# Kernel optimization log

Hardware: AMD Instinct MI355X
Metric: run time of the kernel (lower is better)

## Reference

```python
import math
import jax, jax.numpy as jnp
import numpy as np

B, K, D, R = 8192, 64, 128, 8
EPSILON = 1.0  # alpha_scale, used as diffusion epsilon


def setup_inputs() -> dict:
    key = jax.random.key(0)
    k1, k2, k3 = jax.random.split(key, 3)
    y = jax.random.normal(k1, (B, D), dtype=jnp.float32)
    m = 0.2 * jax.random.normal(k2, (K, D), dtype=jnp.float32)          # init_mean_scale=0.2
    delta = jnp.full((K, D), -2.0, dtype=jnp.float32)                    # init_delta=-2.0
    U = 0.001 * jax.random.normal(k3, (K, D, R), dtype=jnp.float32)
    # log_alpha_raw = alpha_scale * log(ones(K)/K)
    log_alpha_raw = jnp.full((K,), math.log(1.0 / K), dtype=jnp.float32)
    return {"y": y, "m": m, "delta": delta, "U": U, "log_alpha_raw": log_alpha_raw}


def reference(y, m, delta, U, log_alpha_raw):
    """log z_theta(y) = logsumexp_k [log_alpha_k + log N(y; m_k, eps*S_k)],
    S_k = diag(exp(delta_k)) + U_k U_k^T, solved via Woodbury + Cholesky."""
    d = y.shape[-1]
    eps = jnp.asarray(EPSILON, y.dtype)
    log_alpha = (log_alpha_raw - jnp.mean(log_alpha_raw)) / EPSILON

    S_diag = jnp.exp(delta)            # [K, d]
    S_inv = 1.0 / S_diag               # [K, d]

    # Capacitance M_k = I_r + U_k^T diag(S_inv_k) U_k, Cholesky L_k
    V = S_inv[..., None] * U                              # [K, d, r]
    Mcap = jnp.eye(R, dtype=y.dtype) + jnp.einsum('kdr,kds->krs', U, V)  # [K, r, r]
    L = jnp.linalg.cholesky(Mcap)                         # [K, r, r]
    logdet_S = jnp.sum(jnp.log(S_diag), axis=-1) \
        + 2.0 * jnp.sum(jnp.log(jnp.diagonal(L, axis1=-2, axis2=-1)), axis=-1)  # [K]

    diff = y[:, None, :] - m[None, :, :]                  # [B, K, d]
    u1 = diff * S_inv[None]                               # [B, K, d]
    # Woodbury correction: solve M_k s = U_k^T u1 for all (b, k)
    t = jnp.einsum('kdr,bkd->krb', U, u1)                 # [K, r, B] (B as multiple RHS)
    z1 = jax.scipy.linalg.solve_triangular(L, t, lower=True)
    s = jax.scipy.linalg.solve_triangular(jnp.swapaxes(L, -1, -2), z1, lower=False)  # [K, r, B]
    Us = jnp.einsum('kdr,krb->bkd', U, s)                 # [B, K, d]
    S_inv_diff = u1 - Us * S_inv[None]                    # [B, K, d]

    quad = jnp.sum(diff * S_inv_diff, axis=-1)            # [B, K]
    log_norm = 0.5 * (d * (math.log(2.0 * math.pi) + jnp.log(eps)) + logdet_S)  # [K]
    logits = log_alpha[None, :] - 0.5 * quad / eps - log_norm[None, :]          # [B, K]
    return jax.scipy.special.logsumexp(logits, axis=-1)   # [B]
```

## Files before the change

### kernel.cpp

```cpp
#include <hip/hip_runtime.h>
#include <math.h>

#define D_DIM 128
#define K_DIM 64
#define R_DIM 8
#define B_DIM 8192
#define XSTR  264

#define WS_C0F   81920

typedef __bf16 bf16x8 __attribute__((ext_vector_type(8)));
typedef float  f32x4  __attribute__((ext_vector_type(4)));

static __device__ inline unsigned short f2bf(float f) {
  union { float f; unsigned int u; } v; v.f = f;
  unsigned int u = v.u;
  unsigned int lsb = (u >> 16) & 1;
  u += 0x7fffu + lsb;
  return (unsigned short)(u >> 16);
}

__global__ __launch_bounds__(128) void precomp_kernel(
    const float* __restrict__ m, const float* __restrict__ delta,
    const float* __restrict__ U, const float* __restrict__ lar,
    float* __restrict__ ws) {
  const int k = blockIdx.x;
  const int d = threadIdx.x;

  __shared__ float U_l[D_DIM][R_DIM];
  __shared__ float V_l[D_DIM][R_DIM];
  __shared__ float W_l[D_DIM][R_DIM];
  __shared__ float m_l[D_DIM];
  __shared__ float red[64];
  __shared__ float Linv_s[R_DIM][R_DIM];
  __shared__ float q_s[R_DIM];
  __shared__ float c0_s[1];
  __shared__ float redA[D_DIM], redB[D_DIM], redC[D_DIM];

  const float dl    = delta[k * D_DIM + d];
  const float s_inv = expf(-dl);
  const float mv    = m[k * D_DIM + d];
  m_l[d] = mv;
  const float* Up = U + (size_t)(k * D_DIM + d) * R_DIM;
#pragma unroll
  for (int r = 0; r < R_DIM; ++r) {
    float u = Up[r];
    U_l[d][r] = u;
    V_l[d][r] = u * s_inv;
  }
  redA[d] = dl;
  redB[d] = mv * mv * s_inv;
  redC[d] = (d < K_DIM) ? lar[d] : 0.f;
  __syncthreads();

  if (d < 64) {
    const int r = d >> 3, s = d & 7;
    float acc = (r == s) ? 1.0f : 0.0f;
#pragma unroll 8
    for (int dd = 0; dd < D_DIM; ++dd) acc += U_l[dd][r] * V_l[dd][s];
    red[d] = acc;
  }
  __syncthreads();

  for (int off = 64; off > 0; off >>= 1) {
    if (d < off) {
      redA[d] += redA[d + off];
      redB[d] += redB[d + off];
      redC[d] += redC[d + off];
    }
    __syncthreads();
  }

  if (d == 0) {
    float Lm[8][8];
#pragma unroll
    for (int i = 0; i < 8; ++i) {
#pragma unroll
      for (int j = 0; j < 8; ++j) {
        if (j > i) continue;
        float sum = red[i * 8 + j];
#pragma unroll
        for (int p = 0; p < 8; ++p)
          if (p < j) sum -= Lm[i][p] * Lm[j][p];
        if (i == j) Lm[i][i] = sqrtf(sum);
        else        Lm[i][j] = sum / Lm[j][j];
      }
    }
    float ld = 0.f;
#pragma unroll
    for (int i = 0; i < 8; ++i) ld += logf(Lm[i][i]);

    float Li[8][8];
#pragma unroll
    for (int i = 0; i < 8; ++i)
#pragma unroll
      for (int j = 0; j < 8; ++j) Li[i][j] = 0.f;
#pragma unroll
    for (int j = 0; j < 8; ++j) {
      Li[j][j] = 1.0f / Lm[j][j];
#pragma unroll
      for (int i = 0; i < 8; ++i) {
        if (i <= j) continue;
        float sum = 0.f;
#pragma unroll
        for (int p = 0; p < 8; ++p)
          if (p >= j && p < i) sum += Lm[i][p] * Li[p][j];
        Li[i][j] = -sum / Lm[i][i];
      }
    }
#pragma unroll
    for (int i = 0; i < 8; ++i)
#pragma unroll
      for (int j = 0; j < 8; ++j) Linv_s[i][j] = Li[i][j];

    const float mean = redC[0] * (1.0f / K_DIM);
    const float log_alpha = lar[k] - mean;
    const float logdetS = redA[0] + 2.0f * ld;
    const float LOG2PI = 1.8378770664093453f;
    const float log_norm = 0.5f * ((float)D_DIM * LOG2PI + logdetS);
    c0_s[0] = log_alpha - log_norm - 0.5f * redB[0];
  }
  __syncthreads();

  float Wr[R_DIM];
#pragma unroll
  for (int r = 0; r < R_DIM; ++r) {
    float acc = 0.f;
#pragma unroll
    for (int s2 = 0; s2 < R_DIM; ++s2)
      if (s2 <= r) acc += V_l[d][s2] * Linv_s[r][s2];
    Wr[r] = acc;
    W_l[d][r] = acc;
  }
  __syncthreads();

  if (d < R_DIM) {
    float acc = 0.f;
#pragma unroll 8
    for (int dd = 0; dd < D_DIM; ++dd) acc += W_l[dd][d] * m_l[dd];
    q_s[d] = acc;
  }
  __syncthreads();

  float hp = mv * s_inv;
#pragma unroll
  for (int r = 0; r < R_DIM; ++r) hp -= q_s[r] * Wr[r];

  const float INV_SQRT2 = 0.70710678118654752f;
  unsigned short* T = (unsigned short*)ws;
  const int kg = k >> 4, kl = k & 15;
  const int chunk = d >> 5, pos = d & 31;
  const size_t base_y = (((size_t)kg * 8 + chunk) * 160) * 32;
  const size_t base_q = (((size_t)kg * 8 + 4 + chunk) * 160) * 32;
#pragma unroll
  for (int c = 0; c < 8; ++c) {
    T[base_y + (size_t)(kl * 10 + c) * 32 + pos] = f2bf(Wr[c] * INV_SQRT2);
    T[base_q + (size_t)(kl * 10 + c) * 32 + pos] = 0;
  }
  T[base_y + (size_t)(kl * 10 + 8) * 32 + pos] = f2bf(hp);
  T[base_q + (size_t)(kl * 10 + 8) * 32 + pos] = f2bf(-0.5f * s_inv);
  T[base_y + (size_t)(kl * 10 + 9) * 32 + pos] = 0;
  T[base_q + (size_t)(kl * 10 + 9) * 32 + pos] = 0;

  if (d == 0) {
    float qq = 0.f;
#pragma unroll
    for (int r = 0; r < R_DIM; ++r) qq += q_s[r] * q_s[r];
    ws[WS_C0F + k] = c0_s[0] + 0.5f * qq;
  }
}

__global__ __launch_bounds__(512, 1) void logz_full(
    const float* __restrict__ y, const float* __restrict__ ws,
    float* __restrict__ out) {
  __shared__ __align__(16) char smem[16896 + 81920];
  __shared__ float vals2[32 * 65];

  unsigned short* sX = (unsigned short*)smem;
  unsigned short* sT = (unsigned short*)(smem + 16896);

  const int tid   = threadIdx.x;
  const int lane  = tid & 63;
  const int wv    = tid >> 6;
  const int wr    = wv & 1;
  const int wc    = wv >> 1;
  const int col_l = lane & 15;
  const int quad  = lane >> 4;
  const int r0    = (int)blockIdx.x * 32;

  const int kg_m = wv >> 1;
  const int wi5  = (wv & 1) * 5;

  {
#pragma unroll
    for (int j = 0; j < 5; ++j) {
      const int within = wi5 + j;
      const float* src = ws + (size_t)kg_m * 20480 + 0 * 2560 + within * 256;
      __builtin_amdgcn_global_load_lds(
          (const __attribute__((address_space(1))) void*)(src + lane * 4),
          (__attribute__((address_space(3))) void*)(sT + kg_m * 5120 + within * 512),
          16, 0, 0);
    }
  }

  {
#pragma unroll
    for (int j = 0; j < 2; ++j) {
      const int idx = tid + j * 512;
      const int row = idx >> 5, g = idx & 31;
      const float4* ya = (const float4*)y + (size_t)(r0 + row) * 32 + (g & 15) * 2;
      float4 a = ya[0], b = ya[1];
      if (g >= 16) {
        a.x *= a.x; a.y *= a.y; a.z *= a.z; a.w *= a.w;
        b.x *= b.x; b.y *= b.y; b.z *= b.z; b.w *= b.w;
      }
      union { unsigned short us[8]; uint4 v; } o;
      o.us[0] = f2bf(a.x); o.us[1] = f2bf(a.y); o.us[2] = f2bf(a.z); o.us[3] = f2bf(a.w);
      o.us[4] = f2bf(b.x); o.us[5] = f2bf(b.y); o.us[6] = f2bf(b.z); o.us[7] = f2bf(b.w);
      *(uint4*)(sX + row * XSTR + g * 8) = o.v;
    }
  }

  f32x4 acc[10];
#pragma unroll
  for (int f = 0; f < 10; ++f) { acc[f][0] = 0.f; acc[f][1] = 0.f; acc[f][2] = 0.f; acc[f][3] = 0.f; }

  const int rowA = wr * 16 + col_l;

  for (int c = 0; c < 8; ++c) {
    __syncthreads();
    if (c < 7) {
      const int nb = (c + 1) & 1;
#pragma unroll
      for (int j = 0; j < 5; ++j) {
        const int within = wi5 + j;
        const float* src = ws + (size_t)kg_m * 20480 + (c + 1) * 2560 + within * 256;
        __builtin_amdgcn_global_load_lds(
            (const __attribute__((address_space(1))) void*)(src + lane * 4),
            (__attribute__((address_space(3))) void*)(sT + nb * 20480 + kg_m * 5120 + within * 512),
            16, 0, 0);
      }
    }
    const bf16x8 a = *(const bf16x8*)(sX + rowA * XSTR + c * 32 + quad * 8);
    const unsigned short* tb = sT + (c & 1) * 20480 + wc * 5120;
#pragma unroll
    for (int f = 0; f < 10; ++f) {
      const bf16x8 b = *(const bf16x8*)(tb + (f * 16 + col_l) * 32 + quad * 8);
      acc[f] = __builtin_amdgcn_mfma_f32_16x16x32_bf16(a, b, acc[f], 0, 0, 0);
    }
  }

  __syncthreads();
  float* evals = (float*)smem;
#pragma unroll
  for (int f = 0; f < 10; ++f) {
    const int c_in = f * 16 + col_l;
    const int c10  = c_in % 10;
    const int col  = wc * 160 + c_in;
#pragma unroll
    for (int reg = 0; reg < 4; ++reg) {
      const int row = wr * 16 + quad * 4 + reg;
      const float v = acc[f][reg];
      evals[row * 640 + col] = (c10 == 8) ? v : v * v;
    }
  }
  __syncthreads();

  const float* c0p = ws + WS_C0F;
#pragma unroll
  for (int j = 0; j < 4; ++j) {
    const int idx = tid + j * 512;
    const int row = idx >> 6, kl = idx & 63;
    const float* e = evals + row * 640 + kl * 10;
    float s = c0p[kl] + e[8];
#pragma unroll
    for (int c = 0; c < 8; ++c) s += e[c];
    vals2[row * 65 + kl] = s;
  }
  __syncthreads();

#pragma unroll
  for (int rr = 0; rr < 4; ++rr) {
    const int row = wv * 4 + rr;
    const float val = vals2[row * 65 + lane];
    float mx = val;
#pragma unroll
    for (int off = 1; off < 64; off <<= 1)
      mx = fmaxf(mx, __shfl_xor(mx, off, 64));
    float ex = expf(val - mx);
#pragma unroll
    for (int off = 1; off < 64; off <<= 1)
      ex += __shfl_xor(ex, off, 64);
    if (lane == 0) out[r0 + row] = mx + logf(ex);
  }
}

extern "C" void kernel_launch(void* const* d_in, const int* in_sizes, int n_in,
                              void* d_out, int out_size, void* d_ws, size_t ws_size,
                              hipStream_t stream) {
  const float* y     = (const float*)d_in[0];
  const float* m     = (const float*)d_in[1];
  const float* delta = (const float*)d_in[2];
  const float* U     = (const float*)d_in[3];
  const float* lar   = (const float*)d_in[4];
  float* out = (float*)d_out;
  float* ws  = (float*)d_ws;

  precomp_kernel<<<K_DIM, 128, 0, stream>>>(m, delta, U, lar, ws);
  logz_full<<<B_DIM / 32, 512, 0, stream>>>(y, ws, out);
}
```

Baseline: 80.37 us.

## Reorder precomputed B-operand so each MFMA tile holds one feature across 16 components

The precomputed bf16 operand table is relaid out so that each 16-column MFMA fragment holds the same feature (one of 8 projections or the linear term) for 16 mixture components, and the zero padding columns are removed (9 fragments instead of 10). This lets each lane combine squares and the linear term directly in registers, which removes the LDS scatter of the full evaluation matrix, one barrier, and the per-component reduction pass. It also cuts global-to-LDS staging traffic and the MFMA count. The trade-off is a more irregular load loop, with 36 segments spread over 8 waves, so some waves issue an extra load.

```diff
diff --git a/kernel.cpp b/kernel.cpp
--- a/kernel.cpp
+++ b/kernel.cpp
@@ -7,7 +7,7 @@
 #define B_DIM 8192
 #define XSTR  264
 
-#define WS_C0F   81920
+#define WS_C0F   73728
 
 typedef __bf16 bf16x8 __attribute__((ext_vector_type(8)));
 typedef float  f32x4  __attribute__((ext_vector_type(4)));
@@ -150,17 +150,15 @@
   unsigned short* T = (unsigned short*)ws;
   const int kg = k >> 4, kl = k & 15;
   const int chunk = d >> 5, pos = d & 31;
-  const size_t base_y = (((size_t)kg * 8 + chunk) * 160) * 32;
-  const size_t base_q = (((size_t)kg * 8 + 4 + chunk) * 160) * 32;
-#pragma unroll
-  for (int c = 0; c < 8; ++c) {
-    T[base_y + (size_t)(kl * 10 + c) * 32 + pos] = f2bf(Wr[c] * INV_SQRT2);
-    T[base_q + (size_t)(kl * 10 + c) * 32 + pos] = 0;
-  }
-  T[base_y + (size_t)(kl * 10 + 8) * 32 + pos] = f2bf(hp);
-  T[base_q + (size_t)(kl * 10 + 8) * 32 + pos] = f2bf(-0.5f * s_inv);
-  T[base_y + (size_t)(kl * 10 + 9) * 32 + pos] = 0;
-  T[base_q + (size_t)(kl * 10 + 9) * 32 + pos] = 0;
+  const size_t by = (((size_t)(kg * 8 + chunk) * 9) * 16 + kl) * 32 + pos;
+  const size_t bq = (((size_t)(kg * 8 + chunk + 4) * 9) * 16 + kl) * 32 + pos;
+#pragma unroll
+  for (int cc = 0; cc < 8; ++cc) {
+    T[by + (size_t)cc * 512] = f2bf(Wr[cc] * INV_SQRT2);
+    T[bq + (size_t)cc * 512] = 0;
+  }
+  T[by + 8 * 512] = f2bf(hp);
+  T[bq + 8 * 512] = f2bf(-0.5f * s_inv);
 
   if (d == 0) {
     float qq = 0.f;
@@ -173,8 +171,8 @@
 __global__ __launch_bounds__(512, 1) void logz_full(
     const float* __restrict__ y, const float* __restrict__ ws,
     float* __restrict__ out) {
-  __shared__ __align__(16) char smem[16896 + 81920];
-  __shared__ float vals2[32 * 65];
+  __shared__ __align__(16) char smem[16896 + 2 * 36864];
+  __shared__ float vals2[32 * 66];
 
   unsigned short* sX = (unsigned short*)smem;
   unsigned short* sT = (unsigned short*)(smem + 16896);
@@ -188,19 +186,13 @@
   const int quad  = lane >> 4;
   const int r0    = (int)blockIdx.x * 32;
 
-  const int kg_m = wv >> 1;
-  const int wi5  = (wv & 1) * 5;
-
-  {
-#pragma unroll
-    for (int j = 0; j < 5; ++j) {
-      const int within = wi5 + j;
-      const float* src = ws + (size_t)kg_m * 20480 + 0 * 2560 + within * 256;
-      __builtin_amdgcn_global_load_lds(
-          (const __attribute__((address_space(1))) void*)(src + lane * 4),
-          (__attribute__((address_space(3))) void*)(sT + kg_m * 5120 + within * 512),
-          16, 0, 0);
-    }
+  for (int mm = wv; mm < 36; mm += 8) {
+    const int kgm = mm / 9, seg = mm - kgm * 9;
+    const float* src = ws + (size_t)(kgm * 8 + 0) * 2304 + seg * 256 + lane * 4;
+    __builtin_amdgcn_global_load_lds(
+        (const __attribute__((address_space(1))) void*)src,
+        (__attribute__((address_space(3))) void*)(sT + (kgm * 9 + seg) * 512),
+        16, 0, 0);
   }
 
   {
@@ -221,9 +213,9 @@
     }
   }
 
-  f32x4 acc[10];
-#pragma unroll
-  for (int f = 0; f < 10; ++f) { acc[f][0] = 0.f; acc[f][1] = 0.f; acc[f][2] = 0.f; acc[f][3] = 0.f; }
+  f32x4 acc[9];
+#pragma unroll
+  for (int f = 0; f < 9; ++f) { acc[f][0] = 0.f; acc[f][1] = 0.f; acc[f][2] = 0.f; acc[f][3] = 0.f; }
 
   const int rowA = wr * 16 + col_l;
 
@@ -231,58 +223,38 @@
     __syncthreads();
     if (c < 7) {
       const int nb = (c + 1) & 1;
-#pragma unroll
-      for (int j = 0; j < 5; ++j) {
-        const int within = wi5 + j;
-        const float* src = ws + (size_t)kg_m * 20480 + (c + 1) * 2560 + within * 256;
+      for (int mm = wv; mm < 36; mm += 8) {
+        const int kgm = mm / 9, seg = mm - kgm * 9;
+        const float* src = ws + (size_t)(kgm * 8 + c + 1) * 2304 + seg * 256 + lane * 4;
         __builtin_amdgcn_global_load_lds(
-            (const __attribute__((address_space(1))) void*)(src + lane * 4),
-            (__attribute__((address_space(3))) void*)(sT + nb * 20480 + kg_m * 5120 + within * 512),
+            (const __attribute__((address_space(1))) void*)src,
+            (__attribute__((address_space(3))) void*)(sT + nb * 18432 + (kgm * 9 + seg) * 512),
             16, 0, 0);
       }
     }
     const bf16x8 a = *(const bf16x8*)(sX + rowA * XSTR + c * 32 + quad * 8);
-    const unsigned short* tb = sT + (c & 1) * 20480 + wc * 5120;
-#pragma unroll
-    for (int f = 0; f < 10; ++f) {
+    const unsigned short* tb = sT + (c & 1) * 18432 + wc * 4608;
+#pragma unroll
+    for (int f = 0; f < 9; ++f) {
       const bf16x8 b = *(const bf16x8*)(tb + (f * 16 + col_l) * 32 + quad * 8);
       acc[f] = __builtin_amdgcn_mfma_f32_16x16x32_bf16(a, b, acc[f], 0, 0, 0);
     }
   }
 
-  __syncthreads();
-  float* evals = (float*)smem;
-#pragma unroll
-  for (int f = 0; f < 10; ++f) {
-    const int c_in = f * 16 + col_l;
-    const int c10  = c_in % 10;
-    const int col  = wc * 160 + c_in;
-#pragma unroll
-    for (int reg = 0; reg < 4; ++reg) {
-      const int row = wr * 16 + quad * 4 + reg;
-      const float v = acc[f][reg];
-      evals[row * 640 + col] = (c10 == 8) ? v : v * v;
-    }
-  }
-  __syncthreads();
-
-  const float* c0p = ws + WS_C0F;
-#pragma unroll
-  for (int j = 0; j < 4; ++j) {
-    const int idx = tid + j * 512;
-    const int row = idx >> 6, kl = idx & 63;
-    const float* e = evals + row * 640 + kl * 10;
-    float s = c0p[kl] + e[8];
-#pragma unroll
-    for (int c = 0; c < 8; ++c) s += e[c];
-    vals2[row * 65 + kl] = s;
+  const float cv = ws[WS_C0F + wc * 16 + col_l];
+#pragma unroll
+  for (int reg = 0; reg < 4; ++reg) {
+    float v = acc[8][reg];
+#pragma unroll
+    for (int cc = 0; cc < 8; ++cc) v += acc[cc][reg] * acc[cc][reg];
+    vals2[(wr * 16 + quad * 4 + reg) * 66 + wc * 16 + col_l] = cv + v;
   }
   __syncthreads();
 
 #pragma unroll
   for (int rr = 0; rr < 4; ++rr) {
     const int row = wv * 4 + rr;
-    const float val = vals2[row * 65 + lane];
+    const float val = vals2[row * 66 + lane];
     float mx = val;
 #pragma unroll
     for (int off = 1; off < 64; off <<= 1)
```

Measured after the change: 80.32 us. Within noise of the previous version (-0.1%).
